# Optimization experiments

Measured on AMD Instinct MI355X. Metric: run time of the kernel, lower is better.

## Reference

```python
import jax, jax.numpy as jnp
import numpy as np

EPS = 1e-5


def _conv1x1(w, x):
    # w: [O, C, 1, 1], x: [B, C, H, W] -> [B, O, H, W]
    return jnp.einsum('oc,bchw->bohw', w[:, :, 0, 0], x)


def _bn_train(y, g, b):
    # BatchNorm2d in training mode: batch statistics over (B, H, W)
    m = y.mean(axis=(0, 2, 3), keepdims=True)
    v = y.var(axis=(0, 2, 3), keepdims=True)
    return (y - m) * jax.lax.rsqrt(v + EPS) * g[None, :, None, None] + b[None, :, None, None]


def setup_inputs() -> dict:
    key = jax.random.key(0)
    ks = jax.random.split(key, 8)
    B, C, H, W = 16, 512, 32, 32
    width, heads, hd, out_ch = 128, 4, 32, 512  # out_chans*expansion = 512
    return {
        'x': jax.random.normal(ks[0], (B, C, H, W), jnp.float32),
        'conv1_w': jax.random.normal(ks[1], (width, C, 1, 1), jnp.float32) * 0.05,
        'bn1_g': jnp.ones((width,), jnp.float32),
        'bn1_b': jnp.zeros((width,), jnp.float32),
        'qkv_w': jax.random.normal(ks[2], (3 * width, width, 1, 1), jnp.float32) * 0.05,
        'rw': jax.random.normal(ks[3], (1, heads, hd, 1, W), jnp.float32),
        'rh': jax.random.normal(ks[4], (1, heads, hd, H, 1), jnp.float32),
        'conv2_w': jax.random.normal(ks[5], (out_ch, width, 1, 1), jnp.float32) * 0.05,
        'bn2_g': jnp.ones((out_ch,), jnp.float32),
        'bn2_b': jnp.zeros((out_ch,), jnp.float32),
    }


def reference(x, conv1_w, bn1_g, bn1_b, qkv_w, rw, rh, conv2_w, bn2_g, bn2_b):
    B, C, H, W = x.shape
    heads = rw.shape[1]
    width = qkv_w.shape[1]
    hd = width // heads
    scale = hd ** (-0.5)
    N = H * W

    identity = x
    # conv1 = BaseConv: 1x1 conv (no bias) + BN + ReLU
    y = jax.nn.relu(_bn_train(_conv1x1(conv1_w, x), bn1_g, bn1_b))

    # Attention with relative position bias
    qkv = _conv1x1(qkv_w, y)                       # [B, 3*width, H, W]
    qkv = qkv.reshape(B, 3, heads, hd, N)          # split channels as (3, heads, hd)
    q, k, v = qkv[:, 0], qkv[:, 1], qkv[:, 2]      # each [B, heads, hd, N]

    attn_content = jnp.einsum('bhdn,bhdm->bhnm', q, k) * scale  # [B, heads, N, N]
    r = (rw + rh).reshape(heads, hd, N)                          # [heads, hd, N]
    attn_position = jnp.einsum('bhdn,hdm->bhnm', q, r) * scale
    attn = jax.nn.softmax(attn_content + attn_position, axis=-1)
    out = jnp.einsum('bhnm,bhdm->bhdn', attn, v)   # [B, heads, hd, N]
    y = out.reshape(B, width, H, W)

    # conv2 + BN, residual add, ReLU (stride==1: no pooling, no down_sample)
    y = _bn_train(_conv1x1(conv2_w, y), bn2_g, bn2_b)
    y = y + identity
    return jax.nn.relu(y)
```

## Files before the change

kernel.cpp:

```cpp
#include <hip/hip_runtime.h>
#include <cstddef>
#include <cstdint>

constexpr int BATCH = 16;
constexpr int NQ    = 1024;
constexpr float QSCALE = 0.17677669529663687f * 1.4426950408889634f;

typedef __attribute__((ext_vector_type(8))) short bf8;
typedef __attribute__((ext_vector_type(4))) float f32x4;
typedef __attribute__((ext_vector_type(2))) unsigned short us2;
typedef __attribute__((ext_vector_type(4))) unsigned short us4;
typedef __attribute__((ext_vector_type(8))) unsigned short us8;

__device__ inline unsigned short f2bf(float x) {
  union { float f; uint32_t u; } c{x};
  uint32_t r = c.u + 0x7fffu + ((c.u >> 16) & 1u);
  return (unsigned short)(r >> 16);
}
__device__ inline float b2f(unsigned short v) {
  union { uint32_t u; float f; } c{(uint32_t)v << 16};
  return c.f;
}
__device__ inline float fast_exp2(float x) {
#if __has_builtin(__builtin_amdgcn_exp2f)
  return __builtin_amdgcn_exp2f(x);
#else
  return exp2f(x);
#endif
}

__global__ __launch_bounds__(256) void k_wcvt(const float* __restrict__ w1,
                                              const float* __restrict__ wq,
                                              const float* __restrict__ w2,
                                              unsigned short* __restrict__ o1,
                                              unsigned short* __restrict__ oq,
                                              unsigned short* __restrict__ o2) {
  int idx = (blockIdx.x * 256 + threadIdx.x) * 8;
  const float* s; unsigned short* d; int off;
  if (idx < 65536)        { s = w1; d = o1; off = idx; }
  else if (idx < 114688)  { s = wq; d = oq; off = idx - 65536; }
  else                    { s = w2; d = o2; off = idx - 114688; }
  float4 a = *(const float4*)(s + off);
  float4 b = *(const float4*)(s + off + 4);
  us8 o = {f2bf(a.x), f2bf(a.y), f2bf(a.z), f2bf(a.w),
           f2bf(b.x), f2bf(b.y), f2bf(b.z), f2bf(b.w)};
  *(us8*)(d + off) = o;
}

__global__ __launch_bounds__(256) void k_conv1(const float* __restrict__ x,
                                               const unsigned short* __restrict__ W,
                                               unsigned short* __restrict__ y1T,
                                               float* __restrict__ pS1,
                                               float* __restrict__ pQ1) {
  constexpr int BS = 68;
  __shared__ unsigned short Bl[32 * BS];
  __shared__ float Sl[128], Ql[128];

  const int bb = blockIdx.z;
  const int n0 = blockIdx.x * 32;
  const int tid = threadIdx.x, lane = tid & 63;
  const int wm = tid >> 6;
  const int i = lane & 15, g = lane >> 4;

  const int kb = tid >> 3;
  const int nb = tid & 7;

  f32x4 acc[2][2];
#pragma unroll
  for (int a = 0; a < 2; ++a)
#pragma unroll
    for (int b = 0; b < 2; ++b) acc[a][b] = {0.f, 0.f, 0.f, 0.f};

  float4 rv[2];
#pragma unroll
  for (int r = 0; r < 2; ++r)
    rv[r] = *(const float4*)(x + (((size_t)(bb * 512 + kb * 2 + r)) << 10) + n0 + nb * 4);

  for (int s = 0; s < 8; ++s) {
    bf8 wf[2][2];
#pragma unroll
    for (int b = 0; b < 2; ++b)
#pragma unroll
      for (int h = 0; h < 2; ++h)
        wf[b][h] = *(const bf8*)(W + (size_t)(wm * 32 + b * 16 + i) * 512 + s * 64 + h * 32 + g * 8);

    __syncthreads();
#pragma unroll
    for (int j = 0; j < 4; ++j) {
      us2 pk = {f2bf((&rv[0].x)[j]), f2bf((&rv[1].x)[j])};
      *(us2*)&Bl[(nb * 4 + j) * BS + kb * 2] = pk;
    }
    __syncthreads();

    if (s < 7) {
#pragma unroll
      for (int r = 0; r < 2; ++r)
        rv[r] = *(const float4*)(x + (((size_t)(bb * 512 + (s + 1) * 64 + kb * 2 + r)) << 10) + n0 + nb * 4);
    }

#pragma unroll
    for (int h = 0; h < 2; ++h) {
      bf8 af[2];
#pragma unroll
      for (int a = 0; a < 2; ++a)
        af[a] = *(const bf8*)&Bl[(a * 16 + i) * BS + h * 32 + g * 8];
#pragma unroll
      for (int a = 0; a < 2; ++a)
#pragma unroll
        for (int b = 0; b < 2; ++b)
          acc[a][b] = __builtin_amdgcn_mfma_f32_16x16x32_bf16(wf[b][h], af[a], acc[a][b], 0, 0, 0);
    }
  }

#pragma unroll
  for (int a = 0; a < 2; ++a)
#pragma unroll
    for (int b = 0; b < 2; ++b) {
      const int n = n0 + a * 16 + i;
      const int c = wm * 32 + b * 16 + 4 * g;
      us4 pk = {f2bf(acc[a][b][0]), f2bf(acc[a][b][1]), f2bf(acc[a][b][2]), f2bf(acc[a][b][3])};
      *(us4*)(y1T + ((size_t)(bb << 10) + n) * 128 + c) = pk;
    }

#pragma unroll
  for (int b = 0; b < 2; ++b) {
    float sb[4], qb[4];
#pragma unroll
    for (int r = 0; r < 4; ++r) {
      float v0 = b2f(f2bf(acc[0][b][r]));
      float v1 = b2f(f2bf(acc[1][b][r]));
      sb[r] = v0 + v1;
      qb[r] = v0 * v0 + v1 * v1;
    }
#pragma unroll
    for (int o = 1; o < 16; o <<= 1) {
#pragma unroll
      for (int r = 0; r < 4; ++r) {
        sb[r] += __shfl_xor(sb[r], o);
        qb[r] += __shfl_xor(qb[r], o);
      }
    }
    if (i == 0) {
#pragma unroll
      for (int r = 0; r < 4; ++r) {
        const int c = wm * 32 + b * 16 + 4 * g + r;
        Sl[c] = sb[r];
        Ql[c] = qb[r];
      }
    }
  }

  __syncthreads();
  const int blk = bb * 32 + blockIdx.x;
  if (tid < 128) {
    pS1[(size_t)tid * 512 + blk] = Sl[tid];
    pQ1[(size_t)tid * 512 + blk] = Ql[tid];
  }
}

__global__ __launch_bounds__(64) void k_bnfin1(const float* __restrict__ pS1,
                                               const float* __restrict__ pQ1,
                                               const float* __restrict__ g,
                                               const float* __restrict__ be,
                                               float* __restrict__ scl,
                                               float* __restrict__ sht) {
  const int c = blockIdx.x, t = threadIdx.x;
  float S = 0.f, Q = 0.f;
#pragma unroll
  for (int k = 0; k < 8; ++k) {
    S += pS1[(size_t)c * 512 + t + k * 64];
    Q += pQ1[(size_t)c * 512 + t + k * 64];
  }
#pragma unroll
  for (int o = 32; o > 0; o >>= 1) {
    S += __shfl_down(S, o);
    Q += __shfl_down(Q, o);
  }
  if (t == 0) {
    const float inv_n = 1.f / 16384.f;
    const float mean = S * inv_n, var = Q * inv_n - mean * mean;
    const float sc = rsqrtf(var + 1e-5f) * g[c];
    scl[c] = sc;
    sht[c] = be[c] - mean * sc;
  }
}

__global__ __launch_bounds__(256) void k_qkv(const unsigned short* __restrict__ W,
                                             const unsigned short* __restrict__ Bact,
                                             const float* __restrict__ scl,
                                             const float* __restrict__ sht,
                                             const float* __restrict__ rw,
                                             const float* __restrict__ rh,
                                             unsigned short* __restrict__ out0,
                                             unsigned short* __restrict__ out1,
                                             unsigned short* __restrict__ out2) {
  constexpr int BS = 136;
  __shared__ unsigned short Blds[128 * BS];
  __shared__ float scl_s[128], sht_s[128];

  const int bb = blockIdx.z, half = blockIdx.y;
  const int n0 = blockIdx.x * 128;
  const int tid = threadIdx.x, lane = tid & 63, wv = tid >> 6;
  const int wn = wv & 1, wm = wv >> 1;
  const int i = lane & 15, g = lane >> 4;

  const unsigned short* Bp = Bact + ((size_t)bb * NQ + n0) * 128;

  const int sn = tid >> 1;
  const int sk = (tid & 1) * 8;

  if (tid < 128) { scl_s[tid] = scl[tid]; sht_s[tid] = sht[tid]; }

  auto loadw = [&](bf8 (&wf)[2][4], int typ) {
    const int m0 = typ * 128 + half * 64;
#pragma unroll
    for (int b = 0; b < 2; ++b)
#pragma unroll
      for (int h = 0; h < 4; ++h)
        wf[b][h] = *(const bf8*)(W + (size_t)(m0 + wm * 32 + b * 16 + i) * 128 + h * 32 + g * 8);
  };

  bf8 wf0[2][4], wf1[2][4];
  loadw(wf0, 0);
  __syncthreads();

#pragma unroll
  for (int p = 0; p < 8; ++p) {
    us8 v = *(const us8*)(Bp + (size_t)sn * 128 + sk + p * 16);
    const int kb = sk + p * 16;
    float scv[8], shv[8];
    *(float4*)scv = *(const float4*)&scl_s[kb];
    *(float4*)(scv + 4) = *(const float4*)&scl_s[kb + 4];
    *(float4*)shv = *(const float4*)&sht_s[kb];
    *(float4*)(shv + 4) = *(const float4*)&sht_s[kb + 4];
#pragma unroll
    for (int j = 0; j < 8; ++j)
      v[j] = f2bf(fmaxf(fmaf(b2f(v[j]), scv[j], shv[j]), 0.f));
    *(us8*)(&Blds[sn * BS + sk + p * 16]) = v;
  }
  __syncthreads();

  f32x4 acc[4][2];

  auto gemmWA = [&](bf8 (&wf)[2][4]) {
#pragma unroll
    for (int a = 0; a < 4; ++a)
#pragma unroll
      for (int b = 0; b < 2; ++b) acc[a][b] = {0.f, 0.f, 0.f, 0.f};
#pragma unroll
    for (int h = 0; h < 4; ++h) {
      bf8 af[4];
#pragma unroll
      for (int a = 0; a < 4; ++a)
        af[a] = *(const bf8*)&Blds[(wn * 64 + a * 16 + i) * BS + h * 32 + g * 8];
#pragma unroll
      for (int a = 0; a < 4; ++a)
#pragma unroll
        for (int b = 0; b < 2; ++b)
          acc[a][b] = __builtin_amdgcn_mfma_f32_16x16x32_bf16(wf[b][h], af[a], acc[a][b], 0, 0, 0);
    }
  };
  auto gemmAW = [&](bf8 (&wf)[2][4]) {
#pragma unroll
    for (int a = 0; a < 4; ++a)
#pragma unroll
      for (int b = 0; b < 2; ++b) acc[a][b] = {0.f, 0.f, 0.f, 0.f};
#pragma unroll
    for (int h = 0; h < 4; ++h) {
      bf8 af[4];
#pragma unroll
      for (int a = 0; a < 4; ++a)
        af[a] = *(const bf8*)&Blds[(wn * 64 + a * 16 + i) * BS + h * 32 + g * 8];
#pragma unroll
      for (int a = 0; a < 4; ++a)
#pragma unroll
        for (int b = 0; b < 2; ++b)
          acc[a][b] = __builtin_amdgcn_mfma_f32_16x16x32_bf16(af[a], wf[b][h], acc[a][b], 0, 0, 0);
    }
  };

  loadw(wf1, 1);
  gemmWA(wf0);
#pragma unroll
  for (int a = 0; a < 4; ++a)
#pragma unroll
    for (int b = 0; b < 2; ++b) {
      const int n = n0 + wn * 64 + a * 16 + i;
      const int c = half * 64 + wm * 32 + b * 16 + 4 * g;
      const int hh = c >> 5, d = c & 31;
      us4 pk = {f2bf(acc[a][b][0] * QSCALE), f2bf(acc[a][b][1] * QSCALE),
                f2bf(acc[a][b][2] * QSCALE), f2bf(acc[a][b][3] * QSCALE)};
      *(us4*)(out0 + (((size_t)(bb * 4 + hh) << 10) + n) * 32 + d) = pk;
    }

  loadw(wf0, 2);
  gemmWA(wf1);
#pragma unroll
  for (int a = 0; a < 4; ++a)
#pragma unroll
    for (int b = 0; b < 2; ++b) {
      const int n = n0 + wn * 64 + a * 16 + i;
      const int c = half * 64 + wm * 32 + b * 16 + 4 * g;
      const int hh = c >> 5, d = c & 31;
      const int wcol = n & 31, hrow = n >> 5;
      float vv[4];
#pragma unroll
      for (int r = 0; r < 4; ++r)
        vv[r] = acc[a][b][r] + rw[(c + r) * 32 + wcol] + rh[(c + r) * 32 + hrow];
      us4 pk = {f2bf(vv[0]), f2bf(vv[1]), f2bf(vv[2]), f2bf(vv[3])};
      *(us4*)(out1 + (((size_t)(bb * 4 + hh) << 10) + n) * 32 + d) = pk;
    }

  gemmAW(wf0);
#pragma unroll
  for (int a = 0; a < 4; ++a)
#pragma unroll
    for (int b = 0; b < 2; ++b) {
      const int c = half * 64 + wm * 32 + b * 16 + i;
      const int nb = n0 + wn * 64 + a * 16 + 4 * g;
      const int hh = c >> 5, dd = c & 31;
      us4 pk = {f2bf(acc[a][b][0]), f2bf(acc[a][b][1]), f2bf(acc[a][b][2]), f2bf(acc[a][b][3])};
      *(us4*)(out2 + (((size_t)(bb * 4 + hh) * 32 + dd) << 10) + nb) = pk;
    }
}

__global__ __launch_bounds__(256) void k_attn_mfma(const unsigned short* __restrict__ qs,
                                                   const unsigned short* __restrict__ kt,
                                                   const unsigned short* __restrict__ vt,
                                                   float* __restrict__ aoT) {
  const int bh   = blockIdx.y;
  const int tid  = threadIdx.x;
  const int lane = tid & 63;
  const int wv   = tid >> 6;
  const int i    = lane & 15;
  const int g    = lane >> 4;
  const int n0w  = blockIdx.x * 128 + wv * 32;

  __shared__ unsigned short Ks[64 * 56];
  __shared__ unsigned short Vt[32 * 72];

  const bf8 qfA = *(const bf8*)(qs + ((size_t)bh * NQ + n0w + i) * 32 + g * 8);
  const bf8 qfB = *(const bf8*)(qs + ((size_t)bh * NQ + n0w + 16 + i) * 32 + g * 8);

  f32x4 o0A = {0.f,0.f,0.f,0.f}, o1A = {0.f,0.f,0.f,0.f};
  f32x4 o0B = {0.f,0.f,0.f,0.f}, o1B = {0.f,0.f,0.f,0.f};
  float mA = -1e30f, lA = 0.f, mB = -1e30f, lB = 0.f;

  const unsigned short* kb = kt + (size_t)bh * NQ * 32;
  const unsigned short* vb = vt + (size_t)bh * 32 * NQ;

  const int skey = tid >> 2, sds = (tid & 3) * 8;
  const int svd  = tid >> 3, svn = (tid & 7) * 8;

  bf8 kvld = *(const bf8*)(kb + (size_t)skey * 32 + sds);
  bf8 vvld = *(const bf8*)(vb + (size_t)svd * NQ + svn);

  for (int k0 = 0; k0 < NQ; k0 += 64) {
    __syncthreads();
    *(bf8*)&Ks[skey * 56 + sds] = kvld;
    *(bf8*)&Vt[svd * 72 + svn]  = vvld;
    __syncthreads();
    if (k0 + 64 < NQ) {
      kvld = *(const bf8*)(kb + (size_t)(k0 + 64 + skey) * 32 + sds);
      vvld = *(const bf8*)(vb + (size_t)svd * NQ + (k0 + 64) + svn);
    }

    const f32x4 zero = {0.f,0.f,0.f,0.f};
    f32x4 stA[4], stB[4];
#pragma unroll
    for (int t = 0; t < 4; ++t) {
      bf8 kf = *(const bf8*)&Ks[(t * 16 + i) * 56 + g * 8];
      stA[t] = __builtin_amdgcn_mfma_f32_16x16x32_bf16(kf, qfA, zero, 0, 0, 0);
      stB[t] = __builtin_amdgcn_mfma_f32_16x16x32_bf16(kf, qfB, zero, 0, 0, 0);
    }

    unsigned int pkA[4][2], pkB[4][2];
    {
      float tmax = stA[0][0];
#pragma unroll
      for (int t = 0; t < 4; ++t)
#pragma unroll
        for (int r = 0; r < 4; ++r) tmax = fmaxf(tmax, stA[t][r]);
      tmax = fmaxf(tmax, __shfl_xor(tmax, 16));
      tmax = fmaxf(tmax, __shfl_xor(tmax, 32));
      const float mn = fmaxf(mA, tmax);
      const float corr = fast_exp2(mA - mn);
      mA = mn;
      float ps = 0.f;
#pragma unroll
      for (int t = 0; t < 4; ++t) {
        float p0 = fast_exp2(stA[t][0] - mn);
        float p1 = fast_exp2(stA[t][1] - mn);
        float p2 = fast_exp2(stA[t][2] - mn);
        float p3 = fast_exp2(stA[t][3] - mn);
        ps += (p0 + p1) + (p2 + p3);
        unsigned int pa, pb;
        asm("v_cvt_pk_bf16_f32 %0, %1, %2" : "=v"(pa) : "v"(p0), "v"(p1));
        asm("v_cvt_pk_bf16_f32 %0, %1, %2" : "=v"(pb) : "v"(p2), "v"(p3));
        pkA[t][0] = pa; pkA[t][1] = pb;
      }
      ps += __shfl_xor(ps, 16);
      ps += __shfl_xor(ps, 32);
      lA = lA * corr + ps;
#pragma unroll
      for (int r = 0; r < 4; ++r) { o0A[r] *= corr; o1A[r] *= corr; }
    }
    {
      float tmax = stB[0][0];
#pragma unroll
      for (int t = 0; t < 4; ++t)
#pragma unroll
        for (int r = 0; r < 4; ++r) tmax = fmaxf(tmax, stB[t][r]);
      tmax = fmaxf(tmax, __shfl_xor(tmax, 16));
      tmax = fmaxf(tmax, __shfl_xor(tmax, 32));
      const float mn = fmaxf(mB, tmax);
      const float corr = fast_exp2(mB - mn);
      mB = mn;
      float ps = 0.f;
#pragma unroll
      for (int t = 0; t < 4; ++t) {
        float p0 = fast_exp2(stB[t][0] - mn);
        float p1 = fast_exp2(stB[t][1] - mn);
        float p2 = fast_exp2(stB[t][2] - mn);
        float p3 = fast_exp2(stB[t][3] - mn);
        ps += (p0 + p1) + (p2 + p3);
        unsigned int pa, pb;
        asm("v_cvt_pk_bf16_f32 %0, %1, %2" : "=v"(pa) : "v"(p0), "v"(p1));
        asm("v_cvt_pk_bf16_f32 %0, %1, %2" : "=v"(pb) : "v"(p2), "v"(p3));
        pkB[t][0] = pa; pkB[t][1] = pb;
      }
      ps += __shfl_xor(ps, 16);
      ps += __shfl_xor(ps, 32);
      lB = lB * corr + ps;
#pragma unroll
      for (int r = 0; r < 4; ++r) { o0B[r] *= corr; o1B[r] *= corr; }
    }

    const int src0 = ((g & 1) << 5) + i;
    const int src1 = src0 + 16;
    const bool hi = (g >= 2);
#pragma unroll
    for (int s = 0; s < 2; ++s) {
      int a0 = __shfl((int)pkA[2 * s][0], src0);
      int a1 = __shfl((int)pkA[2 * s][1], src0);
      int a2 = __shfl((int)pkA[2 * s][0], src1);
      int a3 = __shfl((int)pkA[2 * s][1], src1);
      int b0 = __shfl((int)pkA[2 * s + 1][0], src0);
      int b1 = __shfl((int)pkA[2 * s + 1][1], src0);
      int b2 = __shfl((int)pkA[2 * s + 1][0], src1);
      int b3 = __shfl((int)pkA[2 * s + 1][1], src1);
      union { int d[4]; bf8 v; } pfA;
      pfA.d[0] = hi ? b0 : a0;
      pfA.d[1] = hi ? b1 : a1;
      pfA.d[2] = hi ? b2 : a2;
      pfA.d[3] = hi ? b3 : a3;
      int c0 = __shfl((int)pkB[2 * s][0], src0);
      int c1 = __shfl((int)pkB[2 * s][1], src0);
      int c2 = __shfl((int)pkB[2 * s][0], src1);
      int c3 = __shfl((int)pkB[2 * s][1], src1);
      int d0 = __shfl((int)pkB[2 * s + 1][0], src0);
      int d1 = __shfl((int)pkB[2 * s + 1][1], src0);
      int d2 = __shfl((int)pkB[2 * s + 1][0], src1);
      int d3 = __shfl((int)pkB[2 * s + 1][1], src1);
      union { int d[4]; bf8 v; } pfB;
      pfB.d[0] = hi ? d0 : c0;
      pfB.d[1] = hi ? d1 : c1;
      pfB.d[2] = hi ? d2 : c2;
      pfB.d[3] = hi ? d3 : c3;
      bf8 vf0 = *(const bf8*)&Vt[(i)      * 72 + s * 32 + g * 8];
      bf8 vf1 = *(const bf8*)&Vt[(16 + i) * 72 + s * 32 + g * 8];
      o0A = __builtin_amdgcn_mfma_f32_16x16x32_bf16(vf0, pfA.v, o0A, 0, 0, 0);
      o1A = __builtin_amdgcn_mfma_f32_16x16x32_bf16(vf1, pfA.v, o1A, 0, 0, 0);
      o0B = __builtin_amdgcn_mfma_f32_16x16x32_bf16(vf0, pfB.v, o0B, 0, 0, 0);
      o1B = __builtin_amdgcn_mfma_f32_16x16x32_bf16(vf1, pfB.v, o1B, 0, 0, 0);
    }
  }

  const float invA = 1.f / lA;
  const float invB = 1.f / lB;
  float* dstA = aoT + (((size_t)(bh >> 2) << 10) + n0w + i) * 128 + (bh & 3) * 32 + 4 * g;
  float* dstB = aoT + (((size_t)(bh >> 2) << 10) + n0w + 16 + i) * 128 + (bh & 3) * 32 + 4 * g;
  f32x4 pA0 = {o0A[0] * invA, o0A[1] * invA, o0A[2] * invA, o0A[3] * invA};
  f32x4 pA1 = {o1A[0] * invA, o1A[1] * invA, o1A[2] * invA, o1A[3] * invA};
  f32x4 pB0 = {o0B[0] * invB, o0B[1] * invB, o0B[2] * invB, o0B[3] * invB};
  f32x4 pB1 = {o1B[0] * invB, o1B[1] * invB, o1B[2] * invB, o1B[3] * invB};
  *(f32x4*)dstA        = pA0;
  *(f32x4*)(dstA + 16) = pA1;
  *(f32x4*)dstB        = pB0;
  *(f32x4*)(dstB + 16) = pB1;
}

__global__ __launch_bounds__(256) void k_stat2(const unsigned short* __restrict__ W,
                                               const float* __restrict__ Aof,
                                               float* __restrict__ pBS,
                                               float* __restrict__ pBQ) {
  constexpr int BS = 264;
  __shared__ unsigned short Blds[64 * BS];
  __shared__ float Sl[256], Ql[256];
  const int bb = blockIdx.z;
  const int mh = blockIdx.y;
  const int n0 = blockIdx.x * 64;
  const int tid = threadIdx.x, lane = tid & 63, wv = tid >> 6;
  const int wn = wv & 1, wm = wv >> 1;
  const int i = lane & 15, g = lane >> 4;

  Sl[tid] = 0.f; Ql[tid] = 0.f;

  const int sn = tid >> 2, sk = (tid & 3) * 32;
  const float* src = Aof + (((size_t)(bb << 10)) + n0 + sn) * 128 + sk;
#pragma unroll
  for (int p = 0; p < 4; ++p) {
    float4 f0 = *(const float4*)(src + p * 8);
    float4 f1 = *(const float4*)(src + p * 8 + 4);
    float fv[8] = {f0.x, f0.y, f0.z, f0.w, f1.x, f1.y, f1.z, f1.w};
    us8 hi, lo;
#pragma unroll
    for (int j = 0; j < 8; ++j) {
      unsigned short h16 = f2bf(fv[j]);
      hi[j] = h16;
      lo[j] = f2bf(fv[j] - b2f(h16));
    }
    *(us8*)&Blds[sn * BS + sk + p * 8]       = hi;
    *(us8*)&Blds[sn * BS + 128 + sk + p * 8] = lo;
  }
  __syncthreads();

  auto loadw = [&](bf8 (&wf)[2][4], int lp) {
    const int mt = mh * 4 + lp;
#pragma unroll
    for (int b = 0; b < 2; ++b)
#pragma unroll
      for (int h = 0; h < 4; ++h)
        wf[b][h] = *(const bf8*)(W + (size_t)(mt * 64 + wm * 32 + b * 16 + i) * 128 + h * 32 + g * 8);
  };

  auto step = [&](bf8 (&wf)[2][4], int lp) {
    f32x4 acc[2][2];
#pragma unroll
    for (int a = 0; a < 2; ++a)
#pragma unroll
      for (int b = 0; b < 2; ++b) acc[a][b] = {0.f, 0.f, 0.f, 0.f};
#pragma unroll
    for (int h = 0; h < 4; ++h) {
      bf8 ah[2], al[2];
#pragma unroll
      for (int a = 0; a < 2; ++a) {
        ah[a] = *(const bf8*)&Blds[(wn * 32 + a * 16 + i) * BS + h * 32 + g * 8];
        al[a] = *(const bf8*)&Blds[(wn * 32 + a * 16 + i) * BS + 128 + h * 32 + g * 8];
      }
#pragma unroll
      for (int a = 0; a < 2; ++a)
#pragma unroll
        for (int b = 0; b < 2; ++b) {
          acc[a][b] = __builtin_amdgcn_mfma_f32_16x16x32_bf16(ah[a], wf[b][h], acc[a][b], 0, 0, 0);
          acc[a][b] = __builtin_amdgcn_mfma_f32_16x16x32_bf16(al[a], wf[b][h], acc[a][b], 0, 0, 0);
        }
    }
#pragma unroll
    for (int b = 0; b < 2; ++b) {
      float s = 0.f, q = 0.f;
#pragma unroll
      for (int a = 0; a < 2; ++a)
#pragma unroll
        for (int r = 0; r < 4; ++r) {
          float v = acc[a][b][r];
          s += v; q += v * v;
        }
      s += __shfl_xor(s, 16); s += __shfl_xor(s, 32);
      q += __shfl_xor(q, 16); q += __shfl_xor(q, 32);
      if ((lane & 48) == 0) {
        const int cl = lp * 64 + wm * 32 + b * 16 + i;
        atomicAdd(&Sl[cl], s);
        atomicAdd(&Ql[cl], q);
      }
    }
  };

  bf8 wfA[2][4], wfB[2][4];
  loadw(wfA, 0);
  loadw(wfB, 1);
  step(wfA, 0);
  loadw(wfA, 2);
  step(wfB, 1);
  loadw(wfB, 3);
  step(wfA, 2);
  step(wfB, 3);

  __syncthreads();
  const int pidx = bb * 16 + blockIdx.x;
  pBS[(size_t)(mh * 256 + tid) * 256 + pidx] = Sl[tid];
  pBQ[(size_t)(mh * 256 + tid) * 256 + pidx] = Ql[tid];
}

__global__ __launch_bounds__(64) void k_bnfin2(const float* __restrict__ pBS,
                                               const float* __restrict__ pBQ,
                                               const float* __restrict__ g,
                                               const float* __restrict__ be,
                                               float* __restrict__ scl,
                                               float* __restrict__ sht) {
  const int c = blockIdx.x, t = threadIdx.x;
  float S = 0.f, Q = 0.f;
#pragma unroll
  for (int k = 0; k < 4; ++k) {
    S += pBS[(size_t)c * 256 + t + k * 64];
    Q += pBQ[(size_t)c * 256 + t + k * 64];
  }
#pragma unroll
  for (int o = 32; o > 0; o >>= 1) {
    S += __shfl_down(S, o);
    Q += __shfl_down(Q, o);
  }
  if (t == 0) {
    const float inv_n = 1.f / 16384.f;
    const float mean = S * inv_n, var = Q * inv_n - mean * mean;
    const float sc = rsqrtf(var + 1e-5f) * g[c];
    scl[c] = sc;
    sht[c] = be[c] - mean * sc;
  }
}

__global__ __launch_bounds__(256) void k_final2(const unsigned short* __restrict__ W,
                                                const float* __restrict__ Aof,
                                                const float* __restrict__ x,
                                                const float* __restrict__ scl2,
                                                const float* __restrict__ sht2,
                                                float* __restrict__ out) {
  constexpr int BS = 264;
  __shared__ unsigned short Blds[64 * BS];
  __shared__ float scl_s[256], sht_s[256];
  const int bb = blockIdx.z;
  const int mh = blockIdx.y;
  const int n0 = blockIdx.x * 64;
  const int tid = threadIdx.x, lane = tid & 63, wv = tid >> 6;
  const int wn = wv & 1, wm = wv >> 1;
  const int i = lane & 15, g = lane >> 4;

  scl_s[tid] = scl2[mh * 256 + tid];
  sht_s[tid] = sht2[mh * 256 + tid];

  const int sn = tid >> 2, sk = (tid & 3) * 32;
  const float* src = Aof + (((size_t)(bb << 10)) + n0 + sn) * 128 + sk;
#pragma unroll
  for (int p = 0; p < 4; ++p) {
    float4 f0 = *(const float4*)(src + p * 8);
    float4 f1 = *(const float4*)(src + p * 8 + 4);
    float fv[8] = {f0.x, f0.y, f0.z, f0.w, f1.x, f1.y, f1.z, f1.w};
    us8 hi, lo;
#pragma unroll
    for (int j = 0; j < 8; ++j) {
      unsigned short h16 = f2bf(fv[j]);
      hi[j] = h16;
      lo[j] = f2bf(fv[j] - b2f(h16));
    }
    *(us8*)&Blds[sn * BS + sk + p * 8]       = hi;
    *(us8*)&Blds[sn * BS + 128 + sk + p * 8] = lo;
  }
  __syncthreads();

  auto loadw = [&](bf8 (&wf)[2][4], int lp) {
    const int mt = mh * 4 + lp;
#pragma unroll
    for (int b = 0; b < 2; ++b)
#pragma unroll
      for (int h = 0; h < 4; ++h)
        wf[b][h] = *(const bf8*)(W + (size_t)(mt * 64 + wm * 32 + b * 16 + i) * 128 + h * 32 + g * 8);
  };

  auto step = [&](bf8 (&wf)[2][4], int lp) {
    const int mt = mh * 4 + lp;
    f32x4 acc[2][2];
#pragma unroll
    for (int a = 0; a < 2; ++a)
#pragma unroll
      for (int b = 0; b < 2; ++b) acc[a][b] = {0.f, 0.f, 0.f, 0.f};
#pragma unroll
    for (int h = 0; h < 4; ++h) {
      bf8 ah[2], al[2];
#pragma unroll
      for (int a = 0; a < 2; ++a) {
        ah[a] = *(const bf8*)&Blds[(wn * 32 + a * 16 + i) * BS + h * 32 + g * 8];
        al[a] = *(const bf8*)&Blds[(wn * 32 + a * 16 + i) * BS + 128 + h * 32 + g * 8];
      }
#pragma unroll
      for (int a = 0; a < 2; ++a)
#pragma unroll
        for (int b = 0; b < 2; ++b) {
          acc[a][b] = __builtin_amdgcn_mfma_f32_16x16x32_bf16(ah[a], wf[b][h], acc[a][b], 0, 0, 0);
          acc[a][b] = __builtin_amdgcn_mfma_f32_16x16x32_bf16(al[a], wf[b][h], acc[a][b], 0, 0, 0);
        }
    }
#pragma unroll
    for (int a = 0; a < 2; ++a)
#pragma unroll
      for (int b = 0; b < 2; ++b) {
        const int c = mt * 64 + wm * 32 + b * 16 + i;
        const int cl = lp * 64 + wm * 32 + b * 16 + i;
        const int nb = n0 + wn * 32 + a * 16 + 4 * g;
        const float sc = scl_s[cl], sh = sht_s[cl];
        const size_t off = (((size_t)(bb * 512 + c)) << 10) + nb;
        float4 xv = *(const float4*)(x + off);
        f32x4 o;
        o[0] = fmaxf(acc[a][b][0] * sc + sh + xv.x, 0.f);
        o[1] = fmaxf(acc[a][b][1] * sc + sh + xv.y, 0.f);
        o[2] = fmaxf(acc[a][b][2] * sc + sh + xv.z, 0.f);
        o[3] = fmaxf(acc[a][b][3] * sc + sh + xv.w, 0.f);
        *(f32x4*)(out + off) = o;
      }
  };

  bf8 wfA[2][4], wfB[2][4];
  loadw(wfA, 0);
  loadw(wfB, 1);
  step(wfA, 0);
  loadw(wfA, 2);
  step(wfB, 1);
  loadw(wfB, 3);
  step(wfA, 2);
  step(wfB, 3);
}

extern "C" void kernel_launch(void* const* d_in, const int* in_sizes, int n_in,
                              void* d_out, int out_size, void* d_ws, size_t ws_size,
                              hipStream_t stream) {
  (void)in_sizes; (void)n_in; (void)out_size; (void)ws_size;
  const float* x    = (const float*)d_in[0];
  const float* w1   = (const float*)d_in[1];
  const float* g1   = (const float*)d_in[2];
  const float* b1   = (const float*)d_in[3];
  const float* wqkv = (const float*)d_in[4];
  const float* rw   = (const float*)d_in[5];
  const float* rh   = (const float*)d_in[6];
  const float* w2   = (const float*)d_in[7];
  const float* g2   = (const float*)d_in[8];
  const float* b2   = (const float*)d_in[9];
  float* out = (float*)d_out;
  char* base = (char*)d_ws;

  float*          aoT = (float*)(base);
  unsigned short* y1T = (unsigned short*)(base + (8u  << 20));
  unsigned short* qs  = (unsigned short*)(base + (12u << 20));
  unsigned short* kt  = (unsigned short*)(base + (16u << 20));
  unsigned short* vt  = (unsigned short*)(base + (20u << 20));
  unsigned short* wb1 = (unsigned short*)(base + (24u << 20));
  unsigned short* wbq = wb1 + 65536;
  unsigned short* wb2 = wbq + 49152;
  float* pS1  = (float*)(base + (25u << 20));
  float* pQ1  = pS1 + 65536;
  float* pBS  = pQ1 + 65536;
  float* pBQ  = pBS + 131072;
  float* scl1 = pBQ + 131072;
  float* sht1 = scl1 + 128;
  float* scl2 = sht1 + 128;
  float* sht2 = scl2 + 512;

  k_wcvt<<<88, 256, 0, stream>>>(w1, wqkv, w2, wb1, wbq, wb2);
  k_conv1<<<dim3(32, 1, BATCH), 256, 0, stream>>>(x, wb1, y1T, pS1, pQ1);
  k_bnfin1<<<128, 64, 0, stream>>>(pS1, pQ1, g1, b1, scl1, sht1);
  k_qkv<<<dim3(8, 2, BATCH), 256, 0, stream>>>(wbq, y1T, scl1, sht1,
                                               rw, rh, qs, kt, vt);
  k_attn_mfma<<<dim3(NQ / 128, BATCH * 4), 256, 0, stream>>>(qs, kt, vt, aoT);
  k_stat2<<<dim3(16, 2, BATCH), 256, 0, stream>>>(wb2, aoT, pBS, pBQ);
  k_bnfin2<<<512, 64, 0, stream>>>(pBS, pBQ, g2, b2, scl2, sht2);
  k_final2<<<dim3(16, 2, BATCH), 256, 0, stream>>>(wb2, aoT, x, scl2, sht2, out);
}
```

Before: 101.7 us.

## Split attention over key halves and merge partials in a combine kernel

```diff
diff --git a/kernel.cpp b/kernel.cpp
--- a/kernel.cpp
+++ b/kernel.cpp
@@ -324,11 +324,14 @@
     }
 }
 
-__global__ __launch_bounds__(256) void k_attn_mfma(const unsigned short* __restrict__ qs,
+__global__ __launch_bounds__(256) void k_attn_part(const unsigned short* __restrict__ qs,
                                                    const unsigned short* __restrict__ kt,
                                                    const unsigned short* __restrict__ vt,
-                                                   float* __restrict__ aoT) {
+                                                   float* __restrict__ po,
+                                                   float* __restrict__ pm,
+                                                   float* __restrict__ pl) {
   const int bh   = blockIdx.y;
+  const int part = blockIdx.z;
   const int tid  = threadIdx.x;
   const int lane = tid & 63;
   const int wv   = tid >> 6;
@@ -352,15 +355,17 @@
   const int skey = tid >> 2, sds = (tid & 3) * 8;
   const int svd  = tid >> 3, svn = (tid & 7) * 8;
 
-  bf8 kvld = *(const bf8*)(kb + (size_t)skey * 32 + sds);
-  bf8 vvld = *(const bf8*)(vb + (size_t)svd * NQ + svn);
-
-  for (int k0 = 0; k0 < NQ; k0 += 64) {
+  const int kbeg = part * 512, kend = kbeg + 512;
+
+  bf8 kvld = *(const bf8*)(kb + (size_t)(kbeg + skey) * 32 + sds);
+  bf8 vvld = *(const bf8*)(vb + (size_t)svd * NQ + kbeg + svn);
+
+  for (int k0 = kbeg; k0 < kend; k0 += 64) {
     __syncthreads();
     *(bf8*)&Ks[skey * 56 + sds] = kvld;
     *(bf8*)&Vt[svd * 72 + svn]  = vvld;
     __syncthreads();
-    if (k0 + 64 < NQ) {
+    if (k0 + 64 < kend) {
       kvld = *(const bf8*)(kb + (size_t)(k0 + 64 + skey) * 32 + sds);
       vvld = *(const bf8*)(vb + (size_t)svd * NQ + (k0 + 64) + svn);
     }
@@ -476,18 +481,54 @@
     }
   }
 
-  const float invA = 1.f / lA;
-  const float invB = 1.f / lB;
-  float* dstA = aoT + (((size_t)(bh >> 2) << 10) + n0w + i) * 128 + (bh & 3) * 32 + 4 * g;
-  float* dstB = aoT + (((size_t)(bh >> 2) << 10) + n0w + 16 + i) * 128 + (bh & 3) * 32 + 4 * g;
-  f32x4 pA0 = {o0A[0] * invA, o0A[1] * invA, o0A[2] * invA, o0A[3] * invA};
-  f32x4 pA1 = {o1A[0] * invA, o1A[1] * invA, o1A[2] * invA, o1A[3] * invA};
-  f32x4 pB0 = {o0B[0] * invB, o0B[1] * invB, o0B[2] * invB, o0B[3] * invB};
-  f32x4 pB1 = {o1B[0] * invB, o1B[1] * invB, o1B[2] * invB, o1B[3] * invB};
-  *(f32x4*)dstA        = pA0;
-  *(f32x4*)(dstA + 16) = pA1;
-  *(f32x4*)dstB        = pB0;
-  *(f32x4*)(dstB + 16) = pB1;
+  const size_t pb = ((size_t)(part * 64 + bh) << 10);
+  float* dA = po + (pb + n0w + i) * 32 + 4 * g;
+  float* dB = po + (pb + n0w + 16 + i) * 32 + 4 * g;
+  *(f32x4*)dA        = o0A;
+  *(f32x4*)(dA + 16) = o1A;
+  *(f32x4*)dB        = o0B;
+  *(f32x4*)(dB + 16) = o1B;
+  if (g == 0) {
+    pm[pb + n0w + i]      = mA;
+    pl[pb + n0w + i]      = lA;
+    pm[pb + n0w + 16 + i] = mB;
+    pl[pb + n0w + 16 + i] = lB;
+  }
+}
+
+__global__ __launch_bounds__(256) void k_attn_comb(const float* __restrict__ po,
+                                                   const float* __restrict__ pm,
+                                                   const float* __restrict__ pl,
+                                                   float* __restrict__ aoT) {
+  const int bh = blockIdx.y;
+  const int q  = blockIdx.x * 64 + (threadIdx.x >> 2);
+  const int dc = (threadIdx.x & 3) * 8;
+
+  const size_t p0 = ((size_t)bh << 10) + q;
+  const size_t p1 = ((size_t)(64 + bh) << 10) + q;
+
+  const float m0 = pm[p0], m1 = pm[p1];
+  const float l0 = pl[p0], l1 = pl[p1];
+  const float M  = fmaxf(m0, m1);
+  const float w0 = fast_exp2(m0 - M);
+  const float w1 = fast_exp2(m1 - M);
+  const float inv = 1.f / (w0 * l0 + w1 * l1);
+  const float c0 = w0 * inv, c1 = w1 * inv;
+
+  f32x4 a0 = *(const f32x4*)(po + p0 * 32 + dc);
+  f32x4 a1 = *(const f32x4*)(po + p0 * 32 + dc + 4);
+  f32x4 b0 = *(const f32x4*)(po + p1 * 32 + dc);
+  f32x4 b1 = *(const f32x4*)(po + p1 * 32 + dc + 4);
+  f32x4 o0, o1;
+#pragma unroll
+  for (int r = 0; r < 4; ++r) {
+    o0[r] = a0[r] * c0 + b0[r] * c1;
+    o1[r] = a1[r] * c0 + b1[r] * c1;
+  }
+
+  float* dst = aoT + (((size_t)(bh >> 2) << 10) + q) * 128 + (bh & 3) * 32 + dc;
+  *(f32x4*)dst       = o0;
+  *(f32x4*)(dst + 4) = o1;
 }
 
 __global__ __launch_bounds__(256) void k_stat2(const unsigned short* __restrict__ W,
@@ -752,13 +793,17 @@
   float* sht1 = scl1 + 128;
   float* scl2 = sht1 + 128;
   float* sht2 = scl2 + 512;
+  float* po   = (float*)(base + (32u << 20));
+  float* pm   = (float*)(base + (48u << 20));
+  float* pl   = pm + 131072;
 
   k_wcvt<<<88, 256, 0, stream>>>(w1, wqkv, w2, wb1, wbq, wb2);
   k_conv1<<<dim3(32, 1, BATCH), 256, 0, stream>>>(x, wb1, y1T, pS1, pQ1);
   k_bnfin1<<<128, 64, 0, stream>>>(pS1, pQ1, g1, b1, scl1, sht1);
   k_qkv<<<dim3(8, 2, BATCH), 256, 0, stream>>>(wbq, y1T, scl1, sht1,
                                                rw, rh, qs, kt, vt);
-  k_attn_mfma<<<dim3(NQ / 128, BATCH * 4), 256, 0, stream>>>(qs, kt, vt, aoT);
+  k_attn_part<<<dim3(NQ / 128, BATCH * 4, 2), 256, 0, stream>>>(qs, kt, vt, po, pm, pl);
+  k_attn_comb<<<dim3(16, BATCH * 4), 256, 0, stream>>>(po, pm, pl, aoT);
   k_stat2<<<dim3(16, 2, BATCH), 256, 0, stream>>>(wb2, aoT, pBS, pBQ);
   k_bnfin2<<<512, 64, 0, stream>>>(pBS, pBQ, g2, b2, scl2, sht2);
   k_final2<<<dim3(16, 2, BATCH), 256, 0, stream>>>(wb2, aoT, x, scl2, sht2, out);
```

Result: no change. 103.3 us (+1.6%).
